# Optimization experiments

Measured on AMD Instinct MI355X. Metric: run time of the kernel, lower is better.

The kernel has to match this reference:

```python
import jax, jax.numpy as jnp
import numpy as np

N_CLUSTERS = 256  # must match fill_max of `clusters`
ALPHA = 7.18
MIN_MEMBERS = 4.0  # clusters with fewer members are dropped (as in original)


def setup_inputs() -> dict:
    key = jax.random.key(0)
    k1, k2 = jax.random.split(key)
    outputs = jax.random.normal(k1, (8192, 2048), dtype=jnp.float32)
    clusters = jax.random.randint(k2, (8192,), 0, N_CLUSTERS, dtype=jnp.int32)
    return {"outputs": outputs, "clusters": clusters}


def _magnet_loss(outputs, clusters):
    # outputs: [N, D] float32, clusters: [N] int32 in [0, N_CLUSTERS)
    n = outputs.shape[0]
    ones = jnp.ones((n,), jnp.float32)
    counts = jax.ops.segment_sum(ones, clusters, num_segments=N_CLUSTERS)          # [C]
    sums = jax.ops.segment_sum(outputs, clusters, num_segments=N_CLUSTERS)         # [C, D]
    means = sums / jnp.maximum(counts, 1.0)[:, None]                               # [C, D]
    valid = counts >= MIN_MEMBERS                                                   # [C] clusters kept
    inst_valid = valid[clusters]                                                    # [N]

    # residual norms to own-cluster mean (UNSQUARED L2, as in original)
    resid = outputs - means[clusters]                                               # [N, D]
    resid_norm = jnp.sqrt(jnp.sum(resid * resid, axis=1))                           # [N]

    num_instances = jnp.sum(jnp.where(valid, counts, 0.0))
    # original quirk: stdev = (sum of norms)^2 / num_instances
    stdev = jnp.square(jnp.sum(jnp.where(inst_valid, resid_norm, 0.0))) / num_instances

    # pairwise instance-to-mean L2 distances via GEMM: [N, C]
    sq = (jnp.sum(outputs * outputs, axis=1)[:, None]
          - 2.0 * (outputs @ means.T)
          + jnp.sum(means * means, axis=1)[None, :])
    dist = jnp.sqrt(jnp.maximum(sq, 0.0))                                           # [N, C]

    expd = jnp.exp(-0.5 * dist / stdev)                                             # [N, C]
    # denominator: sum over valid clusters other than own cluster
    other = jnp.arange(N_CLUSTERS, dtype=clusters.dtype)[None, :] != clusters[:, None]
    mask = valid[None, :] & other                                                   # [N, C]
    denom = jnp.sum(jnp.where(mask, expd, 0.0), axis=1)                             # [N]

    log_num = -0.5 * resid_norm / stdev - ALPHA                                     # [N]
    loss_i = jnp.log(denom) - log_num                                               # -log(exp(log_num)/denom)
    loss = jnp.sum(jnp.where(inst_valid, loss_i, 0.0)) / num_instances
    return loss.reshape(1)


def reference(outputs, clusters):
    return _magnet_loss(outputs.astype(jnp.float32), clusters)
```

## Files before the change

### kernel.cpp

```cpp
#include <hip/hip_runtime.h>
#include <hip/hip_bf16.h>
#include <math.h>

#define NROWS 8192
#define DIM   2048
#define NC    256
#define ALPHA_C 7.18f

typedef float  f32x4  __attribute__((ext_vector_type(4)));
typedef __bf16 bf16x8 __attribute__((ext_vector_type(8)));

#define OFF_A      (size_t)0
#define OFF_DOT    ((size_t)32 << 20)
#define OFF_B      ((size_t)40 << 20)
#define OFF_PERM   ((size_t)41 << 20)
#define OFF_MISC   (OFF_PERM + 32768)
#define OFF_GCTR   (OFF_MISC)
#define OFF_MN2    (OFF_MISC + 1024)
#define OFF_SCAL   (OFF_MISC + 2048)
#define OFF_HIST   (OFF_MISC + 3072)
#define OFF_CNT    (OFF_MISC + 4096)
#define OFF_BASE   (OFF_MISC + 5120)
#define OFF_ON2    (OFF_MISC + 6144)

__device__ __forceinline__ float wave_red_sum(float v) {
#pragma unroll
  for (int off = 32; off > 0; off >>= 1) v += __shfl_xor(v, off, 64);
  return v;
}

__global__ __launch_bounds__(256) void k_hist(const int* __restrict__ clu,
                                              int* __restrict__ hist) {
  __shared__ int h[NC];
  int tid = threadIdx.x;
  h[tid] = 0;
  __syncthreads();
  atomicAdd(&h[clu[blockIdx.x * 256 + tid]], 1);
  __syncthreads();
  if (h[tid]) atomicAdd(&hist[tid], h[tid]);
}

__global__ __launch_bounds__(256) void k_scan(const int* __restrict__ hist,
                                              float* __restrict__ counts,
                                              int* __restrict__ base,
                                              float* scal) {
  __shared__ int pre[NC];
  __shared__ float part[4];
  int tid = threadIdx.x;
  int c = hist[tid];
  counts[tid] = (float)c;
  pre[tid] = c;
  __syncthreads();
  for (int off = 1; off < NC; off <<= 1) {
    int v = (tid >= off) ? pre[tid - off] : 0;
    __syncthreads();
    pre[tid] += v;
    __syncthreads();
  }
  base[tid] = pre[tid] - c;
  float v = (c >= 4) ? (float)c : 0.0f;
  v = wave_red_sum(v);
  if ((tid & 63) == 0) part[tid >> 6] = v;
  __syncthreads();
  if (tid == 0) scal[1] = part[0] + part[1] + part[2] + part[3];
}

__global__ __launch_bounds__(256) void k_perm(const int* __restrict__ clu,
                                              const int* __restrict__ base,
                                              int* __restrict__ gctr,
                                              int* __restrict__ perm) {
  int i = blockIdx.x * 256 + threadIdx.x;
  int c = clu[i];
  int r = atomicAdd(&gctr[c], 1);
  perm[base[c] + r] = i;
}

__global__ __launch_bounds__(256) void k_conv(const float* __restrict__ out,
                                              bf16x8* __restrict__ A,
                                              float* __restrict__ onorm2) {
  __shared__ float lsum[256];
  int mt = blockIdx.x, tid = threadIdx.x;
  int r = tid & 15;
  const float* rowp = out + ((size_t)mt * 16 + r) * DIM;
  bf16x8* At = A + (size_t)mt * 4096;
  float acc = 0.f;
#pragma unroll 4
  for (int s = 0; s < 16; ++s) {
    int q = s * 256 + tid;
    int kk = q >> 6, lane = q & 63;
    int d = kk * 32 + (lane >> 4) * 8;
    const f32x4* src = (const f32x4*)(rowp + d);
    f32x4 v0 = src[0], v1 = src[1];
    bf16x8 b;
#pragma unroll
    for (int j = 0; j < 4; ++j) { float f = v0[j]; acc += f * f; b[j] = (__bf16)f; }
#pragma unroll
    for (int j = 0; j < 4; ++j) { float f = v1[j]; acc += f * f; b[4 + j] = (__bf16)f; }
    At[q] = b;
  }
  lsum[tid] = acc;
  __syncthreads();
  if (tid < 16) {
    float s = 0.f;
#pragma unroll
    for (int k = 0; k < 16; ++k) s += lsum[tid + 16 * k];
    onorm2[mt * 16 + tid] = s;
  }
}

__global__ __launch_bounds__(256) void k_msum(const float* __restrict__ out,
                                              const int* __restrict__ perm,
                                              const int* __restrict__ base,
                                              const float* __restrict__ counts,
                                              __bf16* __restrict__ B,
                                              float* __restrict__ mn2) {
  __shared__ int pr[64];
  __shared__ float part[4];
  int bid = blockIdx.x;
  int c = bid >> 3, sl = bid & 7;
  int tid = threadIdx.x;
  int col = sl * 256 + tid;
  int cnt = (int)counts[c];
  int b0 = base[c];
  float acc = 0.f;
  for (int r0 = 0; r0 < cnt; r0 += 64) {
    int lim = min(64, cnt - r0);
    if (tid < lim) pr[tid] = perm[b0 + r0 + tid];
    __syncthreads();
    for (int r = 0; r < lim; ++r) acc += out[(size_t)pr[r] * DIM + col];
    __syncthreads();
  }
  float mean = acc / fmaxf((float)cnt, 1.f);
  int nt = c >> 4, kk = col >> 5, lane = ((col >> 3) & 3) * 16 + (c & 15), j = col & 7;
  B[(((size_t)nt * 64 + kk) * 64 + lane) * 8 + j] = (__bf16)mean;
  float s = mean * mean;
  s = wave_red_sum(s);
  if ((tid & 63) == 0) part[tid >> 6] = s;
  __syncthreads();
  if (tid == 0) atomicAdd(&mn2[c], part[0] + part[1] + part[2] + part[3]);
}

__global__ __launch_bounds__(256) void k_gemm(const bf16x8* __restrict__ A,
                                              const bf16x8* __restrict__ B,
                                              const int* __restrict__ clu,
                                              const float* __restrict__ counts,
                                              const float* __restrict__ on2v,
                                              const float* __restrict__ mn2,
                                              float* __restrict__ dot,
                                              float* scal) {
  __shared__ float part[4];
  int bid = blockIdx.x;
  int wg = (bid & 7) * 64 + (bid >> 3);
  int bm = wg >> 2, bn = wg & 3;
  int w = threadIdx.x >> 6, l = threadIdx.x & 63;
  int mt = bm * 4 + w;
  int nt0 = bn * 4;
  const bf16x8* Ap = A + (size_t)mt * 4096 + l;
  const bf16x8* Bp = B + (size_t)nt0 * 4096 + l;
  f32x4 acc[4] = {};
#pragma unroll 2
  for (int kk = 0; kk < 64; ++kk) {
    bf16x8 a0 = Ap[kk * 64];
    bf16x8 b0 = Bp[kk * 64];
    bf16x8 b1 = Bp[4096 + kk * 64];
    bf16x8 b2 = Bp[8192 + kk * 64];
    bf16x8 b3 = Bp[12288 + kk * 64];
    acc[0] = __builtin_amdgcn_mfma_f32_16x16x32_bf16(a0, b0, acc[0], 0, 0, 0);
    acc[1] = __builtin_amdgcn_mfma_f32_16x16x32_bf16(a0, b1, acc[1], 0, 0, 0);
    acc[2] = __builtin_amdgcn_mfma_f32_16x16x32_bf16(a0, b2, acc[2], 0, 0, 0);
    acc[3] = __builtin_amdgcn_mfma_f32_16x16x32_bf16(a0, b3, acc[3], 0, 0, 0);
  }
  int r0 = bm * 64 + w * 16 + (l >> 4) * 4;
  int cb = bn * 64 + (l & 15);
#pragma unroll
  for (int reg = 0; reg < 4; ++reg) {
    float* dst = dot + (size_t)(r0 + reg) * NC + cb;
    dst[0]  = acc[0][reg];
    dst[16] = acc[1][reg];
    dst[32] = acc[2][reg];
    dst[48] = acc[3][reg];
  }
  float rsum = 0.f;
#pragma unroll
  for (int reg = 0; reg < 4; ++reg) {
    int i = r0 + reg;
    int ci = clu[i];
#pragma unroll
    for (int n = 0; n < 4; ++n) {
      int c = cb + n * 16;
      if (c == ci && counts[ci] >= 4.0f) {
        rsum += sqrtf(fmaxf(on2v[i] - 2.f * acc[n][reg] + mn2[ci], 0.f));
      }
    }
  }
  rsum = wave_red_sum(rsum);
  if (l == 0) part[w] = rsum;
  __syncthreads();
  if (threadIdx.x == 0) {
    float t = part[0] + part[1] + part[2] + part[3];
    if (t != 0.f) atomicAdd(&scal[0], t);
  }
}

__global__ __launch_bounds__(256) void k_denom(const float* __restrict__ dot,
                                               const int* __restrict__ clu,
                                               const float* __restrict__ on2v,
                                               const float* __restrict__ mn2,
                                               const float* __restrict__ counts,
                                               float* scal) {
  __shared__ float part[4];
  int w = threadIdx.x >> 6, l = threadIdx.x & 63;
  float s0 = scal[0], s1 = scal[1];
  float cfac = -0.5f * s1 / (s0 * s0);
  f32x4 mn = ((const f32x4*)mn2)[l];
  f32x4 cn = ((const f32x4*)counts)[l];
  float lsum = 0.f;
  int i0 = blockIdx.x * 32 + w * 8;
  for (int t = 0; t < 8; ++t) {
    int i = i0 + t;
    int ci = clu[i];
    float on2 = on2v[i];
    f32x4 dv = ((const f32x4*)(dot + (size_t)i * NC))[l];
    float dsum = 0.f;
#pragma unroll
    for (int j = 0; j < 4; ++j) {
      int cc = l * 4 + j;
      float dist = sqrtf(fmaxf(on2 - 2.f * dv[j] + mn[j], 0.f));
      float e = __expf(cfac * dist);
      dsum += ((cn[j] >= 4.0f) && (cc != ci)) ? e : 0.f;
    }
    dsum = wave_red_sum(dsum);
    if (l == 0 && counts[ci] >= 4.0f) {
      float dvi = dot[(size_t)i * NC + ci];
      float rn = sqrtf(fmaxf(on2 - 2.f * dvi + mn2[ci], 0.f));
      lsum += __logf(dsum) - (cfac * rn - ALPHA_C);
    }
  }
  lsum = wave_red_sum(lsum);
  if (l == 0) part[w] = lsum;
  __syncthreads();
  if (threadIdx.x == 0) atomicAdd(&scal[3], part[0] + part[1] + part[2] + part[3]);
}

__global__ void k_final(const float* scal, float* out) {
  out[0] = scal[3] / scal[1];
}

extern "C" void kernel_launch(void* const* d_in, const int* in_sizes, int n_in,
                              void* d_out, int out_size, void* d_ws, size_t ws_size,
                              hipStream_t stream) {
  const float* outputs = (const float*)d_in[0];
  const int* clusters = (const int*)d_in[1];
  float* out = (float*)d_out;
  char* ws = (char*)d_ws;

  bf16x8* A      = (bf16x8*)(ws + OFF_A);
  float*  dotb   = (float*)(ws + OFF_DOT);
  __bf16* B      = (__bf16*)(ws + OFF_B);
  int*    perm   = (int*)(ws + OFF_PERM);
  int*    gctr   = (int*)(ws + OFF_GCTR);
  float*  mn2    = (float*)(ws + OFF_MN2);
  float*  scal   = (float*)(ws + OFF_SCAL);
  int*    hist   = (int*)(ws + OFF_HIST);
  float*  counts = (float*)(ws + OFF_CNT);
  int*    base   = (int*)(ws + OFF_BASE);
  float*  on2    = (float*)(ws + OFF_ON2);

  hipMemsetAsync(ws + OFF_GCTR, 0, 4096, stream);
  k_hist<<<NROWS / 256, 256, 0, stream>>>(clusters, hist);
  k_scan<<<1, 256, 0, stream>>>(hist, counts, base, scal);
  k_perm<<<NROWS / 256, 256, 0, stream>>>(clusters, base, gctr, perm);
  k_conv<<<NROWS / 16, 256, 0, stream>>>(outputs, A, on2);
  k_msum<<<NC * 8, 256, 0, stream>>>(outputs, perm, base, counts, B, mn2);
  k_gemm<<<512, 256, 0, stream>>>(A, (const bf16x8*)B, clusters, counts, on2, mn2, dotb, scal);
  k_denom<<<NROWS / 32, 256, 0, stream>>>(dotb, clusters, on2, mn2, counts, scal);
  k_final<<<1, 1, 0, stream>>>(scal, out);
}
```

Baseline: 172.2 us.

## Split conv, GEMM and denom kernels into more, smaller blocks for occupancy

The bf16 conversion kernel now uses two blocks per 16-row tile and accumulates row norms with atomics into a zeroed buffer. The GEMM uses 1024 blocks, each wave computing a 16x32 tile instead of 16x64. The denominator kernel handles one row per wave, and its partial sums are spread over 32 atomic slots that the final kernel adds up. The aim is to give the MI355X's many CUs more parallel work and to reduce atomic contention on one address, at the cost of more atomics, less operand reuse per wave, and a larger memset.

```diff
diff --git a/kernel.cpp b/kernel.cpp
--- a/kernel.cpp
+++ b/kernel.cpp
@@ -19,9 +19,11 @@
 #define OFF_MN2    (OFF_MISC + 1024)
 #define OFF_SCAL   (OFF_MISC + 2048)
 #define OFF_HIST   (OFF_MISC + 3072)
-#define OFF_CNT    (OFF_MISC + 4096)
-#define OFF_BASE   (OFF_MISC + 5120)
-#define OFF_ON2    (OFF_MISC + 6144)
+#define OFF_LPART  (OFF_MISC + 4096)
+#define OFF_ON2    (OFF_MISC + 5120)
+#define ZSIZE      (5120 + 32768)
+#define OFF_CNT    (OFF_MISC + ZSIZE)
+#define OFF_BASE   (OFF_CNT + 1024)
 
 __device__ __forceinline__ float wave_red_sum(float v) {
 #pragma unroll
@@ -79,24 +81,25 @@
                                               bf16x8* __restrict__ A,
                                               float* __restrict__ onorm2) {
   __shared__ float lsum[256];
-  int mt = blockIdx.x, tid = threadIdx.x;
+  int b = blockIdx.x, tid = threadIdx.x;
+  int mt = b >> 1, half = b & 1;
   int r = tid & 15;
   const float* rowp = out + ((size_t)mt * 16 + r) * DIM;
   bf16x8* At = A + (size_t)mt * 4096;
   float acc = 0.f;
-#pragma unroll 4
-  for (int s = 0; s < 16; ++s) {
-    int q = s * 256 + tid;
+#pragma unroll
+  for (int s2 = 0; s2 < 8; ++s2) {
+    int q = (half * 8 + s2) * 256 + tid;
     int kk = q >> 6, lane = q & 63;
     int d = kk * 32 + (lane >> 4) * 8;
     const f32x4* src = (const f32x4*)(rowp + d);
     f32x4 v0 = src[0], v1 = src[1];
-    bf16x8 b;
-#pragma unroll
-    for (int j = 0; j < 4; ++j) { float f = v0[j]; acc += f * f; b[j] = (__bf16)f; }
-#pragma unroll
-    for (int j = 0; j < 4; ++j) { float f = v1[j]; acc += f * f; b[4 + j] = (__bf16)f; }
-    At[q] = b;
+    bf16x8 bv;
+#pragma unroll
+    for (int j = 0; j < 4; ++j) { float f = v0[j]; acc += f * f; bv[j] = (__bf16)f; }
+#pragma unroll
+    for (int j = 0; j < 4; ++j) { float f = v1[j]; acc += f * f; bv[4 + j] = (__bf16)f; }
+    At[q] = bv;
   }
   lsum[tid] = acc;
   __syncthreads();
@@ -104,7 +107,7 @@
     float s = 0.f;
 #pragma unroll
     for (int k = 0; k < 16; ++k) s += lsum[tid + 16 * k];
-    onorm2[mt * 16 + tid] = s;
+    atomicAdd(&onorm2[mt * 16 + tid], s);
   }
 }
 
@@ -150,47 +153,39 @@
                                               float* scal) {
   __shared__ float part[4];
   int bid = blockIdx.x;
-  int wg = (bid & 7) * 64 + (bid >> 3);
+  int wg = (bid & 7) * 128 + (bid >> 3);
   int bm = wg >> 2, bn = wg & 3;
   int w = threadIdx.x >> 6, l = threadIdx.x & 63;
-  int mt = bm * 4 + w;
-  int nt0 = bn * 4;
+  int wm = w >> 1, wn = w & 1;
+  int mt = bm * 2 + wm;
+  int nt0 = bn * 4 + wn * 2;
   const bf16x8* Ap = A + (size_t)mt * 4096 + l;
   const bf16x8* Bp = B + (size_t)nt0 * 4096 + l;
-  f32x4 acc[4] = {};
-#pragma unroll 2
+  f32x4 acc0 = {}, acc1 = {};
+#pragma unroll 4
   for (int kk = 0; kk < 64; ++kk) {
     bf16x8 a0 = Ap[kk * 64];
     bf16x8 b0 = Bp[kk * 64];
     bf16x8 b1 = Bp[4096 + kk * 64];
-    bf16x8 b2 = Bp[8192 + kk * 64];
-    bf16x8 b3 = Bp[12288 + kk * 64];
-    acc[0] = __builtin_amdgcn_mfma_f32_16x16x32_bf16(a0, b0, acc[0], 0, 0, 0);
-    acc[1] = __builtin_amdgcn_mfma_f32_16x16x32_bf16(a0, b1, acc[1], 0, 0, 0);
-    acc[2] = __builtin_amdgcn_mfma_f32_16x16x32_bf16(a0, b2, acc[2], 0, 0, 0);
-    acc[3] = __builtin_amdgcn_mfma_f32_16x16x32_bf16(a0, b3, acc[3], 0, 0, 0);
-  }
-  int r0 = bm * 64 + w * 16 + (l >> 4) * 4;
-  int cb = bn * 64 + (l & 15);
+    acc0 = __builtin_amdgcn_mfma_f32_16x16x32_bf16(a0, b0, acc0, 0, 0, 0);
+    acc1 = __builtin_amdgcn_mfma_f32_16x16x32_bf16(a0, b1, acc1, 0, 0, 0);
+  }
+  int r0 = bm * 32 + wm * 16 + (l >> 4) * 4;
+  int cb = bn * 64 + wn * 32 + (l & 15);
 #pragma unroll
   for (int reg = 0; reg < 4; ++reg) {
     float* dst = dot + (size_t)(r0 + reg) * NC + cb;
-    dst[0]  = acc[0][reg];
-    dst[16] = acc[1][reg];
-    dst[32] = acc[2][reg];
-    dst[48] = acc[3][reg];
+    dst[0]  = acc0[reg];
+    dst[16] = acc1[reg];
   }
   float rsum = 0.f;
 #pragma unroll
   for (int reg = 0; reg < 4; ++reg) {
     int i = r0 + reg;
     int ci = clu[i];
-#pragma unroll
-    for (int n = 0; n < 4; ++n) {
-      int c = cb + n * 16;
-      if (c == ci && counts[ci] >= 4.0f) {
-        rsum += sqrtf(fmaxf(on2v[i] - 2.f * acc[n][reg] + mn2[ci], 0.f));
-      }
+    if (counts[ci] >= 4.0f) {
+      if (cb == ci)      rsum += sqrtf(fmaxf(on2v[i] - 2.f * acc0[reg] + mn2[ci], 0.f));
+      if (cb + 16 == ci) rsum += sqrtf(fmaxf(on2v[i] - 2.f * acc1[reg] + mn2[ci], 0.f));
     }
   }
   rsum = wave_red_sum(rsum);
@@ -207,43 +202,44 @@
                                                const float* __restrict__ on2v,
                                                const float* __restrict__ mn2,
                                                const float* __restrict__ counts,
-                                               float* scal) {
+                                               const float* scal,
+                                               float* __restrict__ lpart) {
   __shared__ float part[4];
   int w = threadIdx.x >> 6, l = threadIdx.x & 63;
   float s0 = scal[0], s1 = scal[1];
   float cfac = -0.5f * s1 / (s0 * s0);
   f32x4 mn = ((const f32x4*)mn2)[l];
   f32x4 cn = ((const f32x4*)counts)[l];
-  float lsum = 0.f;
-  int i0 = blockIdx.x * 32 + w * 8;
-  for (int t = 0; t < 8; ++t) {
-    int i = i0 + t;
-    int ci = clu[i];
-    float on2 = on2v[i];
-    f32x4 dv = ((const f32x4*)(dot + (size_t)i * NC))[l];
-    float dsum = 0.f;
-#pragma unroll
-    for (int j = 0; j < 4; ++j) {
-      int cc = l * 4 + j;
-      float dist = sqrtf(fmaxf(on2 - 2.f * dv[j] + mn[j], 0.f));
-      float e = __expf(cfac * dist);
-      dsum += ((cn[j] >= 4.0f) && (cc != ci)) ? e : 0.f;
-    }
-    dsum = wave_red_sum(dsum);
-    if (l == 0 && counts[ci] >= 4.0f) {
-      float dvi = dot[(size_t)i * NC + ci];
-      float rn = sqrtf(fmaxf(on2 - 2.f * dvi + mn2[ci], 0.f));
-      lsum += __logf(dsum) - (cfac * rn - ALPHA_C);
-    }
-  }
-  lsum = wave_red_sum(lsum);
-  if (l == 0) part[w] = lsum;
-  __syncthreads();
-  if (threadIdx.x == 0) atomicAdd(&scal[3], part[0] + part[1] + part[2] + part[3]);
-}
-
-__global__ void k_final(const float* scal, float* out) {
-  out[0] = scal[3] / scal[1];
+  int i = blockIdx.x * 4 + w;
+  int ci = clu[i];
+  float on2 = on2v[i];
+  f32x4 dv = ((const f32x4*)(dot + (size_t)i * NC))[l];
+  float dsum = 0.f;
+#pragma unroll
+  for (int j = 0; j < 4; ++j) {
+    int cc = l * 4 + j;
+    float dist = sqrtf(fmaxf(on2 - 2.f * dv[j] + mn[j], 0.f));
+    float e = __expf(cfac * dist);
+    dsum += ((cn[j] >= 4.0f) && (cc != ci)) ? e : 0.f;
+  }
+  dsum = wave_red_sum(dsum);
+  float lv = 0.f;
+  if (l == 0 && counts[ci] >= 4.0f) {
+    float dvi = dot[(size_t)i * NC + ci];
+    float rn = sqrtf(fmaxf(on2 - 2.f * dvi + mn2[ci], 0.f));
+    lv = __logf(dsum) - (cfac * rn - ALPHA_C);
+  }
+  if (l == 0) part[w] = lv;
+  __syncthreads();
+  if (threadIdx.x == 0)
+    atomicAdd(&lpart[blockIdx.x & 31], part[0] + part[1] + part[2] + part[3]);
+}
+
+__global__ void k_final(const float* scal, const float* lpart, float* out) {
+  float s = 0.f;
+#pragma unroll
+  for (int k = 0; k < 32; ++k) s += lpart[k];
+  out[0] = s / scal[1];
 }
 
 extern "C" void kernel_launch(void* const* d_in, const int* in_sizes, int n_in,
@@ -262,17 +258,18 @@
   float*  mn2    = (float*)(ws + OFF_MN2);
   float*  scal   = (float*)(ws + OFF_SCAL);
   int*    hist   = (int*)(ws + OFF_HIST);
+  float*  lpart  = (float*)(ws + OFF_LPART);
+  float*  on2    = (float*)(ws + OFF_ON2);
   float*  counts = (float*)(ws + OFF_CNT);
   int*    base   = (int*)(ws + OFF_BASE);
-  float*  on2    = (float*)(ws + OFF_ON2);
-
-  hipMemsetAsync(ws + OFF_GCTR, 0, 4096, stream);
+
+  hipMemsetAsync(ws + OFF_GCTR, 0, ZSIZE, stream);
   k_hist<<<NROWS / 256, 256, 0, stream>>>(clusters, hist);
   k_scan<<<1, 256, 0, stream>>>(hist, counts, base, scal);
   k_perm<<<NROWS / 256, 256, 0, stream>>>(clusters, base, gctr, perm);
-  k_conv<<<NROWS / 16, 256, 0, stream>>>(outputs, A, on2);
+  k_conv<<<NROWS / 8, 256, 0, stream>>>(outputs, A, on2);
   k_msum<<<NC * 8, 256, 0, stream>>>(outputs, perm, base, counts, B, mn2);
-  k_gemm<<<512, 256, 0, stream>>>(A, (const bf16x8*)B, clusters, counts, on2, mn2, dotb, scal);
-  k_denom<<<NROWS / 32, 256, 0, stream>>>(dotb, clusters, on2, mn2, counts, scal);
-  k_final<<<1, 1, 0, stream>>>(scal, out);
-}
+  k_gemm<<<1024, 256, 0, stream>>>(A, (const bf16x8*)B, clusters, counts, on2, mn2, dotb, scal);
+  k_denom<<<NROWS / 4, 256, 0, stream>>>(dotb, clusters, on2, mn2, counts, scal, lpart);
+  k_final<<<1, 1, 0, stream>>>(scal, lpart, out);
+}
```

Measured after the change: 181.5 us. 1.05x slower.
